# Kernel optimization log

Hardware: AMD Instinct MI355X
Metric: run time of the kernel (lower is better)

Reference implementation:

```python
import jax, jax.numpy as jnp
import numpy as np

BLOCK = 16
NUM_HEADS = 12
EMBED = 768
LN_EPS = 1e-6


def setup_inputs() -> dict:
    key = jax.random.key(0)
    ks = jax.random.split(key, 6)
    H = W = 1024
    x = jax.random.normal(ks[0], (H, W), dtype=jnp.float32)
    # Conv2d(1, EMBED, kernel=BLOCK, stride=BLOCK) weights, flattened to [E, b*b]
    proj_w = jax.random.normal(ks[1], (EMBED, BLOCK * BLOCK), dtype=jnp.float32) * 0.02
    proj_b = jax.random.normal(ks[2], (EMBED,), dtype=jnp.float32) * 0.02
    ln_g = jnp.ones((EMBED,), dtype=jnp.float32)
    ln_b = jnp.zeros((EMBED,), dtype=jnp.float32)
    # nn.Linear(E, 3E, bias=False): weight [3E, E]
    qkv_w = jax.random.normal(ks[3], (3 * EMBED, EMBED), dtype=jnp.float32) * 0.02
    return {"x": x, "proj_w": proj_w, "proj_b": proj_b,
            "ln_g": ln_g, "ln_b": ln_b, "qkv_w": qkv_w}


def reference(x, proj_w, proj_b, ln_g, ln_b, qkv_w):
    H, W = x.shape
    b = BLOCK
    # Patch embed: conv with kernel=stride=b on a single-channel image is
    # exactly patchify + matmul. Token order matches flatten(2) (row-major).
    patches = x.reshape(H // b, b, W // b, b).transpose(0, 2, 1, 3)
    patches = patches.reshape((H // b) * (W // b), b * b)      # [N, b*b]
    tok = patches @ proj_w.T + proj_b                          # [N, E]

    # LayerNorm (eps=1e-6)
    mu = jnp.mean(tok, axis=-1, keepdims=True)
    var = jnp.mean(jnp.square(tok - mu), axis=-1, keepdims=True)
    tok = (tok - mu) * jax.lax.rsqrt(var + LN_EPS) * ln_g + ln_b

    # Attention (batch = 1)
    N, C = tok.shape
    h, d = NUM_HEADS, C // NUM_HEADS
    qkv = (tok @ qkv_w.T).reshape(N, 3, h, d)                  # [N, 3, h, d]
    q = qkv[:, 0].transpose(1, 0, 2)                            # [h, N, d]
    k = qkv[:, 1].transpose(1, 0, 2)
    v = qkv[:, 2].transpose(1, 0, 2)
    scale = d ** -0.5
    attn = jax.nn.softmax(jnp.einsum('hnd,hmd->hnm', q, k) * scale, axis=-1)
    out = jnp.einsum('hnm,hmd->hnd', attn, v)                   # [h, N, d]
    out = out.transpose(1, 0, 2).reshape(N, C)                  # [N, C]
    return out[None]                                            # [1, N, C]
```

## Files before the change

kernel.cpp:

```cpp
#include <hip/hip_runtime.h>
#include <hip/hip_bf16.h>

typedef __bf16 bf16_t;
typedef __attribute__((ext_vector_type(8))) __bf16 bf16x8;
typedef __attribute__((ext_vector_type(4))) __bf16 bf16x4;
typedef __attribute__((ext_vector_type(4))) float f32x4;
typedef __attribute__((ext_vector_type(4))) unsigned int uint4v;

#define QSCALE 0.1803368801111204f

static __device__ inline void glds16(const bf16_t* g, bf16_t* l) {
    __builtin_amdgcn_global_load_lds(
        (__attribute__((address_space(1))) const void*)g,
        (__attribute__((address_space(3))) void*)l,
        16, 0, 0);
}

static __device__ inline float hwexp2(float x) {
#if __has_builtin(__builtin_amdgcn_exp2f)
    return __builtin_amdgcn_exp2f(x);
#else
    float r;
    asm("v_exp_f32 %0, %1" : "=v"(r) : "v"(x));
    return r;
#endif
}

static __device__ inline unsigned int pack_trunc(float lo, float hi) {
    return __builtin_amdgcn_perm(__builtin_bit_cast(unsigned int, hi),
                                 __builtin_bit_cast(unsigned int, lo),
                                 0x07060302u);
}

__global__ void cvt_kernel(const float* __restrict__ in, bf16_t* __restrict__ out, int n4) {
    int i = blockIdx.x * 256 + threadIdx.x;
    if (i < n4) {
        float4 v = ((const float4*)in)[i];
        bf16x4 o = {(bf16_t)v.x, (bf16_t)v.y, (bf16_t)v.z, (bf16_t)v.w};
        ((bf16x4*)out)[i] = o;
    }
}

__global__ __launch_bounds__(256) void patch_gemm(const float* __restrict__ x,
                                                  const bf16_t* __restrict__ pw,
                                                  const float* __restrict__ pb,
                                                  float* __restrict__ tok) {
    const int bm = blockIdx.x;
    const int bn = blockIdx.y;
    const int tid = threadIdx.x;

    __shared__ bf16_t At[64][264];
    __shared__ bf16_t Bt[64][264];

    #pragma unroll
    for (int t = 0; t < 16; t++) {
        int linear = tid + t * 256;
        int ml = linear >> 6;
        int kv = (linear & 63) << 2;
        int n = bm * 64 + ml;
        int pr = n >> 6, pc = n & 63;
        int i = kv >> 4, j = kv & 15;
        float4 v = *(const float4*)(x + (pr * 16 + i) * 1024 + pc * 16 + j);
        bf16x4 o = {(bf16_t)v.x, (bf16_t)v.y, (bf16_t)v.z, (bf16_t)v.w};
        *(bf16x4*)(&At[ml][kv]) = o;
    }
    #pragma unroll
    for (int t = 0; t < 8; t++) {
        int linear = tid + t * 256;
        int nl = linear >> 5;
        int kv = (linear & 31) << 3;
        *(int4*)(&Bt[nl][kv]) = *(const int4*)(pw + (size_t)(bn * 64 + nl) * 256 + kv);
    }
    __syncthreads();

    const int lane = tid & 63, wid = tid >> 6, ln = lane & 15, quad = lane >> 4;
    f32x4 acc[4];
    #pragma unroll
    for (int s = 0; s < 4; s++) acc[s] = {0.f, 0.f, 0.f, 0.f};

    #pragma unroll
    for (int kk = 0; kk < 8; kk++) {
        bf16x8 af = *(const bf16x8*)(&At[wid * 16 + ln][kk * 32 + quad * 8]);
        #pragma unroll
        for (int s = 0; s < 4; s++) {
            bf16x8 bfr = *(const bf16x8*)(&Bt[s * 16 + ln][kk * 32 + quad * 8]);
            acc[s] = __builtin_amdgcn_mfma_f32_16x16x32_bf16(af, bfr, acc[s], 0, 0, 0);
        }
    }

    #pragma unroll
    for (int s = 0; s < 4; s++) {
        int e = bn * 64 + s * 16 + ln;
        float bias = pb[e];
        #pragma unroll
        for (int r = 0; r < 4; r++) {
            int m = bm * 64 + wid * 16 + quad * 4 + r;
            tok[(size_t)m * 768 + e] = acc[s][r] + bias;
        }
    }
}

__global__ __launch_bounds__(256) void ln_kernel(const float* __restrict__ tok,
                                                 const float* __restrict__ g,
                                                 const float* __restrict__ b,
                                                 bf16_t* __restrict__ out) {
    const int n = blockIdx.x;
    const int tid = threadIdx.x;
    const float* row = tok + (size_t)n * 768;
    float x0 = row[tid], x1 = row[tid + 256], x2 = row[tid + 512];
    float s = x0 + x1 + x2;
    float s2 = x0 * x0 + x1 * x1 + x2 * x2;
    #pragma unroll
    for (int off = 32; off; off >>= 1) {
        s += __shfl_xor(s, off);
        s2 += __shfl_xor(s2, off);
    }
    __shared__ float ws1[4], ws2[4];
    int wid = tid >> 6;
    if ((tid & 63) == 0) { ws1[wid] = s; ws2[wid] = s2; }
    __syncthreads();
    s = ws1[0] + ws1[1] + ws1[2] + ws1[3];
    s2 = ws2[0] + ws2[1] + ws2[2] + ws2[3];
    float mu = s * (1.f / 768.f);
    float var = s2 * (1.f / 768.f) - mu * mu;
    float r = rsqrtf(var + 1e-6f);
    bf16_t* orow = out + (size_t)n * 768;
    orow[tid]       = (bf16_t)((x0 - mu) * r * g[tid]       + b[tid]);
    orow[tid + 256] = (bf16_t)((x1 - mu) * r * g[tid + 256] + b[tid + 256]);
    orow[tid + 512] = (bf16_t)((x2 - mu) * r * g[tid + 512] + b[tid + 512]);
}

__global__ __launch_bounds__(256) void qkv_gemm(const bf16_t* __restrict__ tokb,
                                                const bf16_t* __restrict__ wq,
                                                bf16_t* __restrict__ qb,
                                                bf16_t* __restrict__ kswz,
                                                bf16_t* __restrict__ vswz) {
    const int bm = blockIdx.x;
    const int bn = blockIdx.y;
    const int tid = threadIdx.x;

    __shared__ bf16_t At[64][72];
    __shared__ bf16_t Bt[64][72];

    const int rl = tid >> 3;
    const int c8 = (tid & 7) * 8;
    const int lane = tid & 63, wid = tid >> 6, ln = lane & 15, quad = lane >> 4;

    f32x4 acc[4];
    #pragma unroll
    for (int s = 0; s < 4; s++) acc[s] = {0.f, 0.f, 0.f, 0.f};

    for (int kb0 = 0; kb0 < 768; kb0 += 64) {
        __syncthreads();
        #pragma unroll
        for (int p = 0; p < 2; p++) {
            int row = rl + p * 32;
            *(int4*)(&At[row][c8]) = *(const int4*)(tokb + (size_t)(bm * 64 + row) * 768 + kb0 + c8);
            *(int4*)(&Bt[row][c8]) = *(const int4*)(wq   + (size_t)(bn * 64 + row) * 768 + kb0 + c8);
        }
        __syncthreads();
        #pragma unroll
        for (int kk = 0; kk < 2; kk++) {
            bf16x8 af = *(const bf16x8*)(&At[wid * 16 + ln][kk * 32 + quad * 8]);
            #pragma unroll
            for (int s = 0; s < 4; s++) {
                bf16x8 bfr = *(const bf16x8*)(&Bt[s * 16 + ln][kk * 32 + quad * 8]);
                acc[s] = __builtin_amdgcn_mfma_f32_16x16x32_bf16(af, bfr, acc[s], 0, 0, 0);
            }
        }
    }

    const int ncol0 = bn * 64;
    const int sidx = ncol0 / 768;
    const int head = (ncol0 % 768) >> 6;
    #pragma unroll
    for (int s = 0; s < 4; s++) {
        int dc = s * 16 + ln;
        #pragma unroll
        for (int r = 0; r < 4; r++) {
            int m = bm * 64 + wid * 16 + quad * 4 + r;
            if (sidx == 0) {
                qb[((size_t)(head * 4096 + m)) * 64 + dc] = (bf16_t)(acc[s][r] * QSCALE);
            } else if (sidx == 1) {
                bf16_t val = (bf16_t)acc[s][r];
                int kt = m >> 6, sb = (m >> 4) & 3, lnk = m & 15;
                int half = dc >> 5, quadk = (dc >> 3) & 3, j = dc & 7;
                int l = quadk * 16 + lnk;
                kswz[((size_t)(head * 64 + kt)) * 4096 + sb * 1024 + half * 512 + l * 8 + j] = val;
            } else {
                bf16_t val = (bf16_t)acc[s][r];
                int kt = m >> 6, keyl = m & 63;
                int sblk = keyl >> 4;
                int mm = sblk >> 1, tb = sblk & 1;
                int w16 = keyl & 15, qv = w16 >> 2, jj = w16 & 3;
                int jp = tb * 4 + jj;
                int db = dc >> 4, lnv = dc & 15;
                int l = qv * 16 + lnv;
                vswz[((size_t)(head * 64 + kt)) * 4096 + ((mm * 4 + db) * 64 + l) * 8 + jp] = val;
            }
        }
    }
}

__global__ __launch_bounds__(256, 2) void attn_partial(const bf16_t* __restrict__ qbuf,
                                                       const bf16_t* __restrict__ kswz,
                                                       const bf16_t* __restrict__ vswz,
                                                       float* __restrict__ raw0,
                                                       float* __restrict__ raw1,
                                                       float* __restrict__ l_part) {
    const int h = blockIdx.y;
    const int chunk = blockIdx.z;
    const int tid = threadIdx.x;
    const int wid = tid >> 6;
    const int lane = tid & 63;
    const int ln = lane & 15, quad = lane >> 4;
    const int q0 = blockIdx.x * 128;

    __shared__ bf16_t Kf[2][4096];
    __shared__ bf16_t Vf[2][4096];

    bf16x8 qf[2][2];
    #pragma unroll
    for (int g = 0; g < 2; g++) {
        const int q0g = q0 + wid * 32 + g * 16;
        const bf16_t* qrow = qbuf + ((size_t)h * 4096 + q0g + ln) * 64;
        qf[g][0] = *(const bf16x8*)(qrow + quad * 8);
        qf[g][1] = *(const bf16x8*)(qrow + 32 + quad * 8);
    }

    bf16x8 ones;
    #pragma unroll
    for (int i = 0; i < 8; i++) ones[i] = (bf16_t)1.0f;

    const bf16_t* kg = kswz + (size_t)h * 64 * 4096 + (size_t)chunk * 32 * 4096;
    const bf16_t* vg = vswz + (size_t)h * 64 * 4096 + (size_t)chunk * 32 * 4096;

    f32x4 accO[2][4];
    f32x4 accL[2];
    #pragma unroll
    for (int g = 0; g < 2; g++) {
        accL[g] = {0.f, 0.f, 0.f, 0.f};
        #pragma unroll
        for (int d = 0; d < 4; d++) accO[g][d] = {0.f, 0.f, 0.f, 0.f};
    }

    auto stage = [&](int tile, int buf) {
        const bf16_t* kt_g = kg + (size_t)tile * 4096;
        const bf16_t* vt_g = vg + (size_t)tile * 4096;
        #pragma unroll
        for (int i = 0; i < 2; i++) {
            glds16(kt_g + wid * 1024 + i * 512 + lane * 8, &Kf[buf][wid * 1024 + i * 512]);
            glds16(vt_g + wid * 1024 + i * 512 + lane * 8, &Vf[buf][wid * 1024 + i * 512]);
        }
    };

    auto compute = [&](const bf16_t* Kb, const bf16_t* Vb) {
        #pragma unroll
        for (int m = 0; m < 2; m++) {
            bf16x8 vf[4];
            #pragma unroll
            for (int db = 0; db < 4; db++)
                vf[db] = *(const bf16x8*)(Vb + m * 2048 + db * 512 + lane * 8);
            bf16x8 kfa0 = *(const bf16x8*)(Kb + (2 * m) * 1024 + lane * 8);
            bf16x8 kfa1 = *(const bf16x8*)(Kb + (2 * m) * 1024 + 512 + lane * 8);
            bf16x8 kfb0 = *(const bf16x8*)(Kb + (2 * m + 1) * 1024 + lane * 8);
            bf16x8 kfb1 = *(const bf16x8*)(Kb + (2 * m + 1) * 1024 + 512 + lane * 8);
            #pragma unroll
            for (int g = 0; g < 2; g++) {
                f32x4 z = {0.f, 0.f, 0.f, 0.f};
                f32x4 SA = __builtin_amdgcn_mfma_f32_16x16x32_bf16(kfa0, qf[g][0], z, 0, 0, 0);
                SA = __builtin_amdgcn_mfma_f32_16x16x32_bf16(kfa1, qf[g][1], SA, 0, 0, 0);
                f32x4 SB = __builtin_amdgcn_mfma_f32_16x16x32_bf16(kfb0, qf[g][0], z, 0, 0, 0);
                SB = __builtin_amdgcn_mfma_f32_16x16x32_bf16(kfb1, qf[g][1], SB, 0, 0, 0);

                float e0 = hwexp2(SA[0]), e1 = hwexp2(SA[1]), e2 = hwexp2(SA[2]), e3 = hwexp2(SA[3]);
                float e4 = hwexp2(SB[0]), e5 = hwexp2(SB[1]), e6 = hwexp2(SB[2]), e7 = hwexp2(SB[3]);
                uint4v u = {pack_trunc(e0, e1), pack_trunc(e2, e3),
                            pack_trunc(e4, e5), pack_trunc(e6, e7)};
                bf16x8 pb = __builtin_bit_cast(bf16x8, u);
                accL[g] = __builtin_amdgcn_mfma_f32_16x16x32_bf16(ones, pb, accL[g], 0, 0, 0);
                #pragma unroll
                for (int db = 0; db < 4; db++)
                    accO[g][db] = __builtin_amdgcn_mfma_f32_16x16x32_bf16(vf[db], pb, accO[g][db], 0, 0, 0);
            }
        }
    };

    stage(0, 0);

    for (int kt = 0; kt < 32; kt += 2) {
        __builtin_amdgcn_s_barrier();
        stage(kt + 1, 1);
        __builtin_amdgcn_s_waitcnt(0x0F74);
        __builtin_amdgcn_s_barrier();
        compute(&Kf[0][0], &Vf[0][0]);
        __builtin_amdgcn_s_barrier();
        if (kt + 2 < 32) {
            stage(kt + 2, 0);
            __builtin_amdgcn_s_waitcnt(0x0F74);
        } else {
            __builtin_amdgcn_s_waitcnt(0x0F70);
        }
        __builtin_amdgcn_s_barrier();
        compute(&Kf[1][0], &Vf[1][0]);
    }

    float* base = chunk ? raw1 : raw0;
    #pragma unroll
    for (int g = 0; g < 2; g++) {
        const int qg = q0 + wid * 32 + g * 16 + ln;
        if (quad == 0) l_part[(size_t)chunk * 49152 + h * 4096 + qg] = accL[g][0];
        float* op = base + (size_t)qg * 768 + h * 64 + quad * 4;
        #pragma unroll
        for (int db = 0; db < 4; db++)
            *(f32x4*)(op + db * 16) = accO[g][db];
    }
}

__global__ __launch_bounds__(256) void norm_kernel(const float* __restrict__ raw0,
                                                   const float* __restrict__ raw1,
                                                   const float* __restrict__ l_part,
                                                   float* __restrict__ out) {
    const int q = blockIdx.x;
    const int tid = threadIdx.x;
    __shared__ float linv[12];
    if (tid < 12)
        linv[tid] = 1.0f / (l_part[tid * 4096 + q] + l_part[49152 + tid * 4096 + q]);
    __syncthreads();
    #pragma unroll
    for (int t = 0; t < 3; t++) {
        int c = tid + t * 256;
        size_t idx = (size_t)q * 768 + c;
        out[idx] = (raw0[idx] + raw1[idx]) * linv[c >> 6];
    }
}

extern "C" void kernel_launch(void* const* d_in, const int* in_sizes, int n_in,
                              void* d_out, int out_size, void* d_ws, size_t ws_size,
                              hipStream_t stream) {
    const float* x      = (const float*)d_in[0];
    const float* proj_w = (const float*)d_in[1];
    const float* proj_b = (const float*)d_in[2];
    const float* ln_g   = (const float*)d_in[3];
    const float* ln_b   = (const float*)d_in[4];
    const float* qkv_w  = (const float*)d_in[5];
    float* out = (float*)d_out;

    char* ws = (char*)d_ws;
    float*  tok_pre = (float*)(ws + 0);
    bf16_t* tok_b   = (bf16_t*)(ws + 12582912);
    bf16_t* pw_b    = (bf16_t*)(ws + 18874368);
    bf16_t* qw_b    = (bf16_t*)(ws + 19267584);
    bf16_t* qbuf    = (bf16_t*)(ws + 22806528);
    bf16_t* kswz    = (bf16_t*)(ws + 29097984);
    bf16_t* vswz    = (bf16_t*)(ws + 35389440);
    float*  raw0    = tok_pre;
    float*  raw1    = out;
    float*  l_part  = (float*)pw_b;

    cvt_kernel<<<192, 256, 0, stream>>>(proj_w, pw_b, 768 * 256 / 4);
    cvt_kernel<<<1728, 256, 0, stream>>>(qkv_w, qw_b, 2304 * 768 / 4);
    patch_gemm<<<dim3(64, 12), 256, 0, stream>>>(x, pw_b, proj_b, tok_pre);
    ln_kernel<<<4096, 256, 0, stream>>>(tok_pre, ln_g, ln_b, tok_b);
    qkv_gemm<<<dim3(64, 36), 256, 0, stream>>>(tok_b, qw_b, qbuf, kswz, vswz);
    attn_partial<<<dim3(32, 12, 2), 256, 0, stream>>>(qbuf, kswz, vswz, raw0, raw1, l_part);
    norm_kernel<<<4096, 256, 0, stream>>>(raw0, raw1, l_part, out);
}
```

Baseline: 192.7 us.

## Enlarge QKV GEMM tiles to 128x128 with direct-to-LDS loads, merge weight conversions

The QKV projection GEMM moves from 64x64 tiles to 128x128 tiles, with each wave computing a 64x64 sub-block of 4x4 MFMA fragments, so each LDS fragment is reused more. Tiles are loaded with global_load_lds directly into unpadded LDS, and the epilogue maps each wave's column half to a separate head. The two fp32-to-bf16 weight conversion launches are merged into one kernel. Costs include more accumulator registers, fewer blocks (576), and possible LDS bank conflicts from the unpadded layout.

```diff
diff --git a/kernel.cpp b/kernel.cpp
--- a/kernel.cpp
+++ b/kernel.cpp
@@ -32,12 +32,20 @@
                                  0x07060302u);
 }
 
-__global__ void cvt_kernel(const float* __restrict__ in, bf16_t* __restrict__ out, int n4) {
+__global__ void cvt2_kernel(const float* __restrict__ a, bf16_t* __restrict__ oa, int na4,
+                            const float* __restrict__ b, bf16_t* __restrict__ ob, int nb4) {
     int i = blockIdx.x * 256 + threadIdx.x;
-    if (i < n4) {
-        float4 v = ((const float4*)in)[i];
+    if (i < na4) {
+        float4 v = ((const float4*)a)[i];
         bf16x4 o = {(bf16_t)v.x, (bf16_t)v.y, (bf16_t)v.z, (bf16_t)v.w};
-        ((bf16x4*)out)[i] = o;
+        ((bf16x4*)oa)[i] = o;
+    } else {
+        int j = i - na4;
+        if (j < nb4) {
+            float4 v = ((const float4*)b)[j];
+            bf16x4 o = {(bf16_t)v.x, (bf16_t)v.y, (bf16_t)v.z, (bf16_t)v.w};
+            ((bf16x4*)ob)[j] = o;
+        }
     }
 }
 
@@ -138,65 +146,78 @@
     const int bm = blockIdx.x;
     const int bn = blockIdx.y;
     const int tid = threadIdx.x;
-
-    __shared__ bf16_t At[64][72];
-    __shared__ bf16_t Bt[64][72];
-
-    const int rl = tid >> 3;
-    const int c8 = (tid & 7) * 8;
-    const int lane = tid & 63, wid = tid >> 6, ln = lane & 15, quad = lane >> 4;
-
-    f32x4 acc[4];
-    #pragma unroll
-    for (int s = 0; s < 4; s++) acc[s] = {0.f, 0.f, 0.f, 0.f};
+    const int wid = tid >> 6, lane = tid & 63;
+    const int ln = lane & 15, quad = lane >> 4;
+    const int wm = wid & 1, wn = wid >> 1;
+
+    __shared__ bf16_t At[128 * 64];
+    __shared__ bf16_t Bt[128 * 64];
+
+    f32x4 acc[4][4];
+    #pragma unroll
+    for (int sm = 0; sm < 4; sm++)
+        #pragma unroll
+        for (int sn = 0; sn < 4; sn++) acc[sm][sn] = {0.f, 0.f, 0.f, 0.f};
+
+    const int srow = wid * 32 + (lane >> 3);
+    const int scol = (lane & 7) * 8;
 
     for (int kb0 = 0; kb0 < 768; kb0 += 64) {
         __syncthreads();
         #pragma unroll
-        for (int p = 0; p < 2; p++) {
-            int row = rl + p * 32;
-            *(int4*)(&At[row][c8]) = *(const int4*)(tokb + (size_t)(bm * 64 + row) * 768 + kb0 + c8);
-            *(int4*)(&Bt[row][c8]) = *(const int4*)(wq   + (size_t)(bn * 64 + row) * 768 + kb0 + c8);
+        for (int i = 0; i < 4; i++) {
+            glds16(tokb + (size_t)(bm * 128 + srow + i * 8) * 768 + kb0 + scol,
+                   At + wid * 2048 + i * 512);
+            glds16(wq + (size_t)(bn * 128 + srow + i * 8) * 768 + kb0 + scol,
+                   Bt + wid * 2048 + i * 512);
         }
         __syncthreads();
         #pragma unroll
         for (int kk = 0; kk < 2; kk++) {
-            bf16x8 af = *(const bf16x8*)(&At[wid * 16 + ln][kk * 32 + quad * 8]);
+            bf16x8 af[4], bfr[4];
             #pragma unroll
             for (int s = 0; s < 4; s++) {
-                bf16x8 bfr = *(const bf16x8*)(&Bt[s * 16 + ln][kk * 32 + quad * 8]);
-                acc[s] = __builtin_amdgcn_mfma_f32_16x16x32_bf16(af, bfr, acc[s], 0, 0, 0);
+                af[s]  = *(const bf16x8*)(At + (wm * 64 + s * 16 + ln) * 64 + kk * 32 + quad * 8);
+                bfr[s] = *(const bf16x8*)(Bt + (wn * 64 + s * 16 + ln) * 64 + kk * 32 + quad * 8);
             }
-        }
-    }
-
-    const int ncol0 = bn * 64;
-    const int sidx = ncol0 / 768;
-    const int head = (ncol0 % 768) >> 6;
-    #pragma unroll
-    for (int s = 0; s < 4; s++) {
-        int dc = s * 16 + ln;
-        #pragma unroll
-        for (int r = 0; r < 4; r++) {
-            int m = bm * 64 + wid * 16 + quad * 4 + r;
-            if (sidx == 0) {
-                qb[((size_t)(head * 4096 + m)) * 64 + dc] = (bf16_t)(acc[s][r] * QSCALE);
-            } else if (sidx == 1) {
-                bf16_t val = (bf16_t)acc[s][r];
-                int kt = m >> 6, sb = (m >> 4) & 3, lnk = m & 15;
-                int half = dc >> 5, quadk = (dc >> 3) & 3, j = dc & 7;
-                int l = quadk * 16 + lnk;
-                kswz[((size_t)(head * 64 + kt)) * 4096 + sb * 1024 + half * 512 + l * 8 + j] = val;
-            } else {
-                bf16_t val = (bf16_t)acc[s][r];
-                int kt = m >> 6, keyl = m & 63;
-                int sblk = keyl >> 4;
-                int mm = sblk >> 1, tb = sblk & 1;
-                int w16 = keyl & 15, qv = w16 >> 2, jj = w16 & 3;
-                int jp = tb * 4 + jj;
-                int db = dc >> 4, lnv = dc & 15;
-                int l = qv * 16 + lnv;
-                vswz[((size_t)(head * 64 + kt)) * 4096 + ((mm * 4 + db) * 64 + l) * 8 + jp] = val;
+            #pragma unroll
+            for (int sm = 0; sm < 4; sm++)
+                #pragma unroll
+                for (int sn = 0; sn < 4; sn++)
+                    acc[sm][sn] = __builtin_amdgcn_mfma_f32_16x16x32_bf16(af[sm], bfr[sn], acc[sm][sn], 0, 0, 0);
+        }
+    }
+
+    const int sidx = bn / 6;
+    const int head = (bn % 6) * 2 + wn;
+    #pragma unroll
+    for (int sn = 0; sn < 4; sn++) {
+        int dc = sn * 16 + ln;
+        #pragma unroll
+        for (int sm = 0; sm < 4; sm++) {
+            #pragma unroll
+            for (int r = 0; r < 4; r++) {
+                int m = bm * 128 + wm * 64 + sm * 16 + quad * 4 + r;
+                float v = acc[sm][sn][r];
+                if (sidx == 0) {
+                    qb[((size_t)(head * 4096 + m)) * 64 + dc] = (bf16_t)(v * QSCALE);
+                } else if (sidx == 1) {
+                    bf16_t val = (bf16_t)v;
+                    int kt = m >> 6, sb = (m >> 4) & 3, lnk = m & 15;
+                    int half = dc >> 5, quadk = (dc >> 3) & 3, j = dc & 7;
+                    int l = quadk * 16 + lnk;
+                    kswz[((size_t)(head * 64 + kt)) * 4096 + sb * 1024 + half * 512 + l * 8 + j] = val;
+                } else {
+                    bf16_t val = (bf16_t)v;
+                    int kt = m >> 6, keyl = m & 63;
+                    int sblk = keyl >> 4;
+                    int mm = sblk >> 1, tb = sblk & 1;
+                    int w16 = keyl & 15, qv = w16 >> 2, jj = w16 & 3;
+                    int jp = tb * 4 + jj;
+                    int db = dc >> 4, lnv = dc & 15;
+                    int l = qv * 16 + lnv;
+                    vswz[((size_t)(head * 64 + kt)) * 4096 + ((mm * 4 + db) * 64 + l) * 8 + jp] = val;
+                }
             }
         }
     }
@@ -358,11 +379,10 @@
     float*  raw1    = out;
     float*  l_part  = (float*)pw_b;
 
-    cvt_kernel<<<192, 256, 0, stream>>>(proj_w, pw_b, 768 * 256 / 4);
-    cvt_kernel<<<1728, 256, 0, stream>>>(qkv_w, qw_b, 2304 * 768 / 4);
+    cvt2_kernel<<<1920, 256, 0, stream>>>(proj_w, pw_b, 49152, qkv_w, qw_b, 442368);
     patch_gemm<<<dim3(64, 12), 256, 0, stream>>>(x, pw_b, proj_b, tok_pre);
     ln_kernel<<<4096, 256, 0, stream>>>(tok_pre, ln_g, ln_b, tok_b);
-    qkv_gemm<<<dim3(64, 36), 256, 0, stream>>>(tok_b, qw_b, qbuf, kswz, vswz);
+    qkv_gemm<<<dim3(32, 18), 256, 0, stream>>>(tok_b, qw_b, qbuf, kswz, vswz);
     attn_partial<<<dim3(32, 12, 2), 256, 0, stream>>>(qbuf, kswz, vswz, raw0, raw1, l_part);
     norm_kernel<<<4096, 256, 0, stream>>>(raw0, raw1, l_part, out);
 }
```

After: 189.1 us. No clear change (-1.9%).
